# Performance work log

Hardware: AMD Instinct MI355X
Metric: run time of the kernel (lower is better)

Reference implementation:

```python
import jax, jax.numpy as jnp
import numpy as np

# Synthetic kinematic tree: 1 root + C0 chains of L0 atoms (generation 0 scans,
# rooted at node 0) + C1 branches of L1 atoms rooted mid-chain (generation 1 scans).
C0, L0 = 2048, 768
C1, L1 = 2048, 256
N = 1 + C0 * L0 + C1 * L1  # 2_097_153 atoms (incl. virtual root)


def setup_inputs() -> dict:
    key = jax.random.key(0)
    dofs = jax.random.normal(key, (N, 9), dtype=jnp.float32)

    chain_starts = 1 + np.arange(C0, dtype=np.int64) * L0          # first atom of each chain
    gen0 = np.concatenate(
        [np.zeros((C0, 1), np.int64),
         chain_starts[:, None] + np.arange(L0)[None, :]], axis=1)    # [C0, L0+1], col0 = root

    branch_roots = chain_starts + L0 // 2                            # computed during gen 0
    boff = 1 + C0 * L0
    gen1 = np.concatenate(
        [branch_roots[:, None],
         boff + (np.arange(C1, dtype=np.int64) * L1)[:, None] + np.arange(L1)[None, :]],
        axis=1)                                                      # [C1, L1+1]

    doftype = np.full((N,), 2, np.int32)  # BOND
    doftype[0] = 0                        # ROOT
    doftype[chain_starts] = 1             # JUMP at each chain start

    # kintree.id[1:] -> coords index: a fixed permutation (irregular scatter)
    id_idx = np.random.default_rng(0).permutation(N - 1).astype(np.int32)

    return {
        "dofs": dofs,
        "doftype": jnp.asarray(doftype),
        "gen0_paths": jnp.asarray(gen0, dtype=jnp.int32),
        "gen1_paths": jnp.asarray(gen1, dtype=jnp.int32),
        "id_idx": jnp.asarray(id_idx),
    }


def _rx(a):
    c, s = jnp.cos(a), jnp.sin(a)
    o, z = jnp.ones_like(a), jnp.zeros_like(a)
    return jnp.stack([jnp.stack([o, z, z, z], -1),
                      jnp.stack([z, c, -s, z], -1),
                      jnp.stack([z, s, c, z], -1),
                      jnp.stack([z, z, z, o], -1)], -2)


def _ry(a):
    c, s = jnp.cos(a), jnp.sin(a)
    o, z = jnp.ones_like(a), jnp.zeros_like(a)
    return jnp.stack([jnp.stack([c, z, s, z], -1),
                      jnp.stack([z, o, z, z], -1),
                      jnp.stack([-s, z, c, z], -1),
                      jnp.stack([z, z, z, o], -1)], -2)


def _rz(a):
    c, s = jnp.cos(a), jnp.sin(a)
    o, z = jnp.ones_like(a), jnp.zeros_like(a)
    return jnp.stack([jnp.stack([c, -s, z, z], -1),
                      jnp.stack([s, c, z, z], -1),
                      jnp.stack([z, z, o, z], -1),
                      jnp.stack([z, z, z, o], -1)], -2)


def _trans(x, y, z):
    o, zr = jnp.ones_like(x), jnp.zeros_like(x)
    return jnp.stack([jnp.stack([o, zr, zr, x], -1),
                      jnp.stack([zr, o, zr, y], -1),
                      jnp.stack([zr, zr, o, z], -1),
                      jnp.stack([zr, zr, zr, o], -1)], -2)


def _local_hts(dofs, doftype):
    # BOND dofs: phi_p, theta, d, phi_c  (NeRF-style internal coordinates)
    phi_p, theta, d, phi_c = dofs[:, 0], dofs[:, 1], dofs[:, 2], dofs[:, 3]
    z = jnp.zeros_like(d)
    bond = _rx(phi_p) @ _rz(jnp.pi - theta) @ _trans(d, z, z) @ _rx(phi_c)
    # JUMP dofs: RBx,RBy,RBz, RBdel_(a,b,c), RB_(a,b,c)
    rot = lambda a, b, c: _rz(c) @ _ry(b) @ _rx(a)
    jump = (_trans(dofs[:, 0], dofs[:, 1], dofs[:, 2])
            @ rot(dofs[:, 3], dofs[:, 4], dofs[:, 5])
            @ rot(dofs[:, 6], dofs[:, 7], dofs[:, 8]))
    eye = jnp.broadcast_to(jnp.eye(4, dtype=dofs.dtype), bond.shape)
    dt = doftype[:, None, None]
    return jnp.where(dt == 1, jump, jnp.where(dt == 2, bond, eye))


def reference(dofs, doftype, gen0_paths, gen1_paths, id_idx):
    hts = _local_hts(dofs, doftype)  # [N, 4, 4] local HTs; root = identity
    # Generation-ordered segmented scan: within each generation, each scan path's
    # first node already holds its GLOBAL HT; compose child = parent @ local along
    # the path via an associative prefix-matmul, then scatter back.
    for paths in (gen0_paths, gen1_paths):
        seg = hts[paths]                                        # [S, Lp, 4, 4]
        scanned = jax.lax.associative_scan(jnp.matmul, seg, axis=1)
        hts = hts.at[paths].set(scanned)
    kincoords = hts[:, :3, 3]                                   # [N, 3]
    coords = jnp.zeros((N - 1, 3), dtype=dofs.dtype)
    coords = coords.at[id_idx].set(kincoords[1:])               # coords[id[1:]] = kincoords[1:]
    return coords
```

## Files before the change

kernel.cpp:

```cpp
#include <hip/hip_runtime.h>
#include <math.h>

#define NC0 2048
#define NL0 768
#define NL1 256
#define BOFF (1 + NC0 * NL0)

struct Aff { float f[12]; };

__device__ __forceinline__ Aff affIdentity() {
    Aff M;
    M.f[0]=1.f; M.f[1]=0.f; M.f[2]=0.f;
    M.f[3]=0.f; M.f[4]=1.f; M.f[5]=0.f;
    M.f[6]=0.f; M.f[7]=0.f; M.f[8]=1.f;
    M.f[9]=0.f; M.f[10]=0.f; M.f[11]=0.f;
    return M;
}

__device__ __forceinline__ Aff compose(const Aff& A, const Aff& B) {
    Aff C;
#pragma unroll
    for (int i = 0; i < 3; ++i) {
        const float a0 = A.f[i*3+0], a1 = A.f[i*3+1], a2 = A.f[i*3+2];
#pragma unroll
        for (int j = 0; j < 3; ++j)
            C.f[i*3+j] = a0*B.f[0*3+j] + a1*B.f[1*3+j] + a2*B.f[2*3+j];
        C.f[9+i] = a0*B.f[9] + a1*B.f[10] + a2*B.f[11] + A.f[9+i];
    }
    return C;
}

__device__ __forceinline__ Aff shflUpA(const Aff& A, int d) {
    Aff B;
#pragma unroll
    for (int k = 0; k < 12; ++k) B.f[k] = __shfl_up(A.f[k], d, 64);
    return B;
}

__device__ __forceinline__ void fsc(float a, float& s, float& c) {
    s = __sinf(a);
    c = __cosf(a);
}

__device__ __forceinline__ Aff bondHT(float phi_p, float theta, float dd, float phi_c) {
    float sp, cp, st, ct, sc, cc;
    fsc(phi_p, sp, cp);
    fsc(theta, st, ct);
    fsc(phi_c, sc, cc);
    const float ca = -ct, sa = st;
    const float r00 = ca,    r01 = -sa;
    const float r10 = cp*sa, r11 = cp*ca,  r12 = -sp;
    const float r20 = sp*sa, r21 = sp*ca,  r22 = cp;
    Aff M;
    M.f[0] = r00; M.f[1] = r01*cc;          M.f[2] = -r01*sc;
    M.f[3] = r10; M.f[4] = r11*cc + r12*sc; M.f[5] = -r11*sc + r12*cc;
    M.f[6] = r20; M.f[7] = r21*cc + r22*sc; M.f[8] = -r21*sc + r22*cc;
    M.f[9] = r00*dd; M.f[10] = r10*dd; M.f[11] = r20*dd;
    return M;
}

__device__ __forceinline__ void rot3(float a, float b, float c, float* R) {
    float sa, ca, sb, cb, sg, cg;
    fsc(a, sa, ca);
    fsc(b, sb, cb);
    fsc(c, sg, cg);
    R[0] = cb*cg; R[1] = sa*sb*cg - ca*sg; R[2] = ca*sb*cg + sa*sg;
    R[3] = cb*sg; R[4] = sa*sb*sg + ca*cg; R[5] = ca*sb*sg - sa*cg;
    R[6] = -sb;   R[7] = sa*cb;            R[8] = ca*cb;
}

__device__ __forceinline__ Aff jumpHT(float d0, float d1, float d2,
                                      float d3, float d4, float d5,
                                      float d6, float d7, float d8) {
    float R1[9], R2[9];
    rot3(d3, d4, d5, R1);
    rot3(d6, d7, d8, R2);
    Aff M;
#pragma unroll
    for (int i = 0; i < 3; ++i)
#pragma unroll
        for (int j = 0; j < 3; ++j)
            M.f[i*3+j] = R1[i*3+0]*R2[0*3+j] + R1[i*3+1]*R2[1*3+j] + R1[i*3+2]*R2[2*3+j];
    M.f[9] = d0; M.f[10] = d1; M.f[11] = d2;
    return M;
}

__device__ __forceinline__ float f4c(const float4 v, int j) {
    return j == 0 ? v.x : j == 1 ? v.y : j == 2 ? v.z : v.w;
}
__device__ __forceinline__ int i4c(const int4 v, int j) {
    return j == 0 ? v.x : j == 1 ? v.y : j == 2 ? v.z : v.w;
}

#define GFA(m) f4c(ch[((m)+1)>>2], ((m)+1)&3)
#define GFB(m) f4c(chb[((m)+1)>>2], ((m)+1)&3)

__global__ __launch_bounds__(64)
void kin_kernel(const float* __restrict__ dofs,
                const int* __restrict__ id_idx,
                float* __restrict__ out) {
    const int c = blockIdx.x;
    const int t = threadIdx.x;

    const int ib0 = c * NL0 + 12 * t;
    const int4 i0 = *(const int4*)(id_idx + ib0 + 0);
    const int4 i1 = *(const int4*)(id_idx + ib0 + 4);
    const int4 i2 = *(const int4*)(id_idx + ib0 + 8);
    const int4 ibv = *(const int4*)(id_idx + (BOFF - 1) + c * NL1 + 4 * t);

    const float4* g4 = (const float4*)dofs;
    const size_t f0  = (size_t)(1 + c * NL0 + 12 * t) * 9;
    const size_t cb0 = (f0 - 1) >> 2;
    float4 ch[26];
    ch[0]  = g4[cb0 + 0];  ch[1]  = g4[cb0 + 1];  ch[2]  = g4[cb0 + 2];
    ch[3]  = g4[cb0 + 3];  ch[4]  = g4[cb0 + 4];  ch[5]  = g4[cb0 + 5];
    ch[7]  = g4[cb0 + 7];  ch[9]  = g4[cb0 + 9];  ch[10] = g4[cb0 + 10];
    ch[11] = g4[cb0 + 11]; ch[12] = g4[cb0 + 12]; ch[13] = g4[cb0 + 13];
    ch[14] = g4[cb0 + 14]; ch[16] = g4[cb0 + 16]; ch[18] = g4[cb0 + 18];
    ch[19] = g4[cb0 + 19]; ch[20] = g4[cb0 + 20]; ch[21] = g4[cb0 + 21];
    ch[22] = g4[cb0 + 22]; ch[23] = g4[cb0 + 23]; ch[25] = g4[cb0 + 25];

    const size_t f1  = (size_t)(BOFF + c * NL1 + 4 * t) * 9;
    const size_t cb1 = (f1 - 1) >> 2;
    float4 chb[8];
    chb[0] = g4[cb1 + 0]; chb[1] = g4[cb1 + 1]; chb[2] = g4[cb1 + 2];
    chb[3] = g4[cb1 + 3]; chb[4] = g4[cb1 + 4]; chb[5] = g4[cb1 + 5];
    chb[7] = g4[cb1 + 7];

    float qx[12], qy[12], qz[12];
    Aff Q, H0f;
#pragma unroll
    for (int k = 0; k < 12; ++k) {
        Aff H;
        if (k == 0) {
            if (t == 0)
                H = jumpHT(GFA(0), GFA(1), GFA(2), GFA(3), GFA(4),
                           GFA(5), GFA(6), GFA(7), GFA(8));
            else
                H = bondHT(GFA(0), GFA(1), GFA(2), GFA(3));
            H0f = H;
            Q = H;
        } else {
            H = bondHT(GFA(9*k+0), GFA(9*k+1), GFA(9*k+2), GFA(9*k+3));
            Q = compose(Q, H);
        }
        qx[k] = Q.f[9]; qy[k] = Q.f[10]; qz[k] = Q.f[11];
    }

    Aff S = Q;
#pragma unroll
    for (int s = 1; s < 64; s <<= 1) {
        const Aff P = shflUpA(S, s);
        if (t >= s) S = compose(P, S);
    }
    Aff E = shflUpA(S, 1);
    if (t == 0) E = affIdentity();

#pragma unroll
    for (int k = 0; k < 12; ++k) {
        const int oi = (k < 4) ? i4c(i0, k) : (k < 8) ? i4c(i1, k - 4) : i4c(i2, k - 8);
        float* o = out + (size_t)oi * 3;
        o[0] = E.f[0]*qx[k] + E.f[1]*qy[k] + E.f[2]*qz[k] + E.f[9];
        o[1] = E.f[3]*qx[k] + E.f[4]*qy[k] + E.f[5]*qz[k] + E.f[10];
        o[2] = E.f[6]*qx[k] + E.f[7]*qy[k] + E.f[8]*qz[k] + E.f[11];
    }

    Aff G = compose(E, H0f);
#pragma unroll
    for (int j = 0; j < 12; ++j) G.f[j] = __shfl(G.f[j], 32, 64);

    float rx[4], ry[4], rz[4];
    Aff R;
#pragma unroll
    for (int k = 0; k < 4; ++k) {
        const Aff Hb = bondHT(GFB(9*k+0), GFB(9*k+1), GFB(9*k+2), GFB(9*k+3));
        R = (k == 0) ? Hb : compose(R, Hb);
        rx[k] = R.f[9]; ry[k] = R.f[10]; rz[k] = R.f[11];
    }

    Aff Sb = R;
#pragma unroll
    for (int s = 1; s < 64; s <<= 1) {
        const Aff P = shflUpA(Sb, s);
        if (t >= s) Sb = compose(P, Sb);
    }
    Aff E1 = shflUpA(Sb, 1);
    if (t == 0) E1 = affIdentity();

    const Aff M = compose(G, E1);
#pragma unroll
    for (int k = 0; k < 4; ++k) {
        const int oi = i4c(ibv, k);
        float* o = out + (size_t)oi * 3;
        o[0] = M.f[0]*rx[k] + M.f[1]*ry[k] + M.f[2]*rz[k] + M.f[9];
        o[1] = M.f[3]*rx[k] + M.f[4]*ry[k] + M.f[5]*rz[k] + M.f[10];
        o[2] = M.f[6]*rx[k] + M.f[7]*ry[k] + M.f[8]*rz[k] + M.f[11];
    }
}

extern "C" void kernel_launch(void* const* d_in, const int* in_sizes, int n_in,
                              void* d_out, int out_size, void* d_ws, size_t ws_size,
                              hipStream_t stream) {
    const float* dofs   = (const float*)d_in[0];
    const int*   id_idx = (const int*)d_in[4];
    float*       out    = (float*)d_out;

    hipLaunchKernelGGL(kin_kernel, dim3(NC0), dim3(64), 0, stream,
                       dofs, id_idx, out);
}
```

Baseline: 163.5 us.

## Split each chain across two waves with LDS carry and interleaved scans

Each block now runs 128 threads (two waves), and each thread handles 6 chain atoms and 2 branch atoms instead of 12 and 4. The two wave-level scans for the chain and the branch are interleaved in one shuffle loop. Wave 0's totals pass to wave 1 through shared memory behind a block barrier. The branch root is rebuilt from wave 0's total times the bond at atom 384, so the broadcast from lane 32 is gone. The aim is to shorten each thread's serial chain and raise parallelism and occupancy, at the cost of a __syncthreads, extra composes, and narrower float2 loads.

```diff
diff --git a/kernel.cpp b/kernel.cpp
--- a/kernel.cpp
+++ b/kernel.cpp
@@ -85,52 +85,68 @@
     return M;
 }
 
-__device__ __forceinline__ float f4c(const float4 v, int j) {
-    return j == 0 ? v.x : j == 1 ? v.y : j == 2 ? v.z : v.w;
-}
-__device__ __forceinline__ int i4c(const int4 v, int j) {
-    return j == 0 ? v.x : j == 1 ? v.y : j == 2 ? v.z : v.w;
-}
-
-#define GFA(m) f4c(ch[((m)+1)>>2], ((m)+1)&3)
-#define GFB(m) f4c(chb[((m)+1)>>2], ((m)+1)&3)
-
-__global__ __launch_bounds__(64)
+__device__ __forceinline__ float f2c(const float2 v, int j) { return j ? v.y : v.x; }
+
+__device__ __forceinline__ void stA12(float* p, const Aff& A) {
+#pragma unroll
+    for (int k = 0; k < 12; ++k) p[k] = A.f[k];
+}
+__device__ __forceinline__ Aff ldA12(const float* p) {
+    Aff A;
+#pragma unroll
+    for (int k = 0; k < 12; ++k) A.f[k] = p[k];
+    return A;
+}
+
+#define GFA(m) f2c(ca[((m)+1)>>1], ((m)+1)&1)
+#define GFB(m) f2c(cb[((m)+1)>>1], ((m)+1)&1)
+#define GFR(m) f2c(cr[((m)+1)>>1], ((m)+1)&1)
+
+__global__ __launch_bounds__(128, 4)
 void kin_kernel(const float* __restrict__ dofs,
                 const int* __restrict__ id_idx,
                 float* __restrict__ out) {
-    const int c = blockIdx.x;
-    const int t = threadIdx.x;
-
-    const int ib0 = c * NL0 + 12 * t;
-    const int4 i0 = *(const int4*)(id_idx + ib0 + 0);
-    const int4 i1 = *(const int4*)(id_idx + ib0 + 4);
-    const int4 i2 = *(const int4*)(id_idx + ib0 + 8);
-    const int4 ibv = *(const int4*)(id_idx + (BOFF - 1) + c * NL1 + 4 * t);
-
-    const float4* g4 = (const float4*)dofs;
-    const size_t f0  = (size_t)(1 + c * NL0 + 12 * t) * 9;
-    const size_t cb0 = (f0 - 1) >> 2;
-    float4 ch[26];
-    ch[0]  = g4[cb0 + 0];  ch[1]  = g4[cb0 + 1];  ch[2]  = g4[cb0 + 2];
-    ch[3]  = g4[cb0 + 3];  ch[4]  = g4[cb0 + 4];  ch[5]  = g4[cb0 + 5];
-    ch[7]  = g4[cb0 + 7];  ch[9]  = g4[cb0 + 9];  ch[10] = g4[cb0 + 10];
-    ch[11] = g4[cb0 + 11]; ch[12] = g4[cb0 + 12]; ch[13] = g4[cb0 + 13];
-    ch[14] = g4[cb0 + 14]; ch[16] = g4[cb0 + 16]; ch[18] = g4[cb0 + 18];
-    ch[19] = g4[cb0 + 19]; ch[20] = g4[cb0 + 20]; ch[21] = g4[cb0 + 21];
-    ch[22] = g4[cb0 + 22]; ch[23] = g4[cb0 + 23]; ch[25] = g4[cb0 + 25];
-
-    const size_t f1  = (size_t)(BOFF + c * NL1 + 4 * t) * 9;
-    const size_t cb1 = (f1 - 1) >> 2;
-    float4 chb[8];
-    chb[0] = g4[cb1 + 0]; chb[1] = g4[cb1 + 1]; chb[2] = g4[cb1 + 2];
-    chb[3] = g4[cb1 + 3]; chb[4] = g4[cb1 + 4]; chb[5] = g4[cb1 + 5];
-    chb[7] = g4[cb1 + 7];
-
-    float qx[12], qy[12], qz[12];
-    Aff Q, H0f;
-#pragma unroll
-    for (int k = 0; k < 12; ++k) {
+    __shared__ float wt0[12];
+    __shared__ float wt1[12];
+
+    const int c    = blockIdx.x;
+    const int t    = threadIdx.x;
+    const int lane = t & 63;
+    const int wave = t >> 6;
+
+    const int ob0 = c * NL0 + 6 * t;
+    const int2 j0 = *(const int2*)(id_idx + ob0 + 0);
+    const int2 j1 = *(const int2*)(id_idx + ob0 + 2);
+    const int2 j2 = *(const int2*)(id_idx + ob0 + 4);
+    const int2 jb = *(const int2*)(id_idx + (BOFF - 1) + c * NL1 + 2 * t);
+
+    const float2* g2 = (const float2*)dofs;
+    const size_t f0 = (size_t)9 * (1 + (size_t)c * NL0 + 6 * t);
+    const size_t p0 = (f0 - 1) >> 1;
+    float2 ca[25];
+    ca[0]  = g2[p0+0];  ca[1]  = g2[p0+1];  ca[2]  = g2[p0+2];
+    ca[3]  = g2[p0+3];  ca[4]  = g2[p0+4];
+    ca[5]  = g2[p0+5];  ca[6]  = g2[p0+6];
+    ca[9]  = g2[p0+9];  ca[10] = g2[p0+10]; ca[11] = g2[p0+11];
+    ca[14] = g2[p0+14]; ca[15] = g2[p0+15];
+    ca[18] = g2[p0+18]; ca[19] = g2[p0+19]; ca[20] = g2[p0+20];
+    ca[23] = g2[p0+23]; ca[24] = g2[p0+24];
+
+    const size_t f1 = (size_t)9 * ((size_t)BOFF + (size_t)c * NL1 + 2 * t);
+    const size_t p1 = (f1 - 1) >> 1;
+    float2 cb[7];
+    cb[0] = g2[p1+0]; cb[1] = g2[p1+1]; cb[2] = g2[p1+2];
+    cb[5] = g2[p1+5]; cb[6] = g2[p1+6];
+
+    const size_t fr = (size_t)9 * (1 + (size_t)c * NL0 + 384);
+    const size_t pr = (fr - 1) >> 1;
+    float2 cr[3];
+    cr[0] = g2[pr+0]; cr[1] = g2[pr+1]; cr[2] = g2[pr+2];
+
+    float qx[6], qy[6], qz[6];
+    Aff Q;
+#pragma unroll
+    for (int k = 0; k < 6; ++k) {
         Aff H;
         if (k == 0) {
             if (t == 0)
@@ -138,7 +154,6 @@
                            GFA(5), GFA(6), GFA(7), GFA(8));
             else
                 H = bondHT(GFA(0), GFA(1), GFA(2), GFA(3));
-            H0f = H;
             Q = H;
         } else {
             H = bondHT(GFA(9*k+0), GFA(9*k+1), GFA(9*k+2), GFA(9*k+3));
@@ -147,50 +162,54 @@
         qx[k] = Q.f[9]; qy[k] = Q.f[10]; qz[k] = Q.f[11];
     }
 
+    float rx[2], ry[2], rz[2];
+    Aff R0 = bondHT(GFB(0), GFB(1), GFB(2), GFB(3));
+    rx[0] = R0.f[9]; ry[0] = R0.f[10]; rz[0] = R0.f[11];
+    Aff Sb = compose(R0, bondHT(GFB(9), GFB(10), GFB(11), GFB(12)));
+    rx[1] = Sb.f[9]; ry[1] = Sb.f[10]; rz[1] = Sb.f[11];
+
     Aff S = Q;
 #pragma unroll
     for (int s = 1; s < 64; s <<= 1) {
-        const Aff P = shflUpA(S, s);
-        if (t >= s) S = compose(P, S);
-    }
+        const Aff A = shflUpA(S, s);
+        const Aff B = shflUpA(Sb, s);
+        if (lane >= s) {
+            S  = compose(A, S);
+            Sb = compose(B, Sb);
+        }
+    }
+    if (wave == 0 && lane == 63) { stA12(wt0, S); stA12(wt1, Sb); }
+    __syncthreads();
+
+    const Aff W0 = ldA12(wt0);
+    const Aff W1 = ldA12(wt1);
+
     Aff E = shflUpA(S, 1);
-    if (t == 0) E = affIdentity();
-
-#pragma unroll
-    for (int k = 0; k < 12; ++k) {
-        const int oi = (k < 4) ? i4c(i0, k) : (k < 8) ? i4c(i1, k - 4) : i4c(i2, k - 8);
+    if (lane == 0) E = affIdentity();
+    const Aff EW = wave ? compose(W0, E) : E;
+
+#pragma unroll
+    for (int k = 0; k < 6; ++k) {
+        const int oi = (k < 2) ? (k ? j0.y : j0.x)
+                     : (k < 4) ? (k == 3 ? j1.y : j1.x)
+                               : (k == 5 ? j2.y : j2.x);
         float* o = out + (size_t)oi * 3;
-        o[0] = E.f[0]*qx[k] + E.f[1]*qy[k] + E.f[2]*qz[k] + E.f[9];
-        o[1] = E.f[3]*qx[k] + E.f[4]*qy[k] + E.f[5]*qz[k] + E.f[10];
-        o[2] = E.f[6]*qx[k] + E.f[7]*qy[k] + E.f[8]*qz[k] + E.f[11];
-    }
-
-    Aff G = compose(E, H0f);
-#pragma unroll
-    for (int j = 0; j < 12; ++j) G.f[j] = __shfl(G.f[j], 32, 64);
-
-    float rx[4], ry[4], rz[4];
-    Aff R;
-#pragma unroll
-    for (int k = 0; k < 4; ++k) {
-        const Aff Hb = bondHT(GFB(9*k+0), GFB(9*k+1), GFB(9*k+2), GFB(9*k+3));
-        R = (k == 0) ? Hb : compose(R, Hb);
-        rx[k] = R.f[9]; ry[k] = R.f[10]; rz[k] = R.f[11];
-    }
-
-    Aff Sb = R;
-#pragma unroll
-    for (int s = 1; s < 64; s <<= 1) {
-        const Aff P = shflUpA(Sb, s);
-        if (t >= s) Sb = compose(P, Sb);
-    }
+        o[0] = EW.f[0]*qx[k] + EW.f[1]*qy[k] + EW.f[2]*qz[k] + EW.f[9];
+        o[1] = EW.f[3]*qx[k] + EW.f[4]*qy[k] + EW.f[5]*qz[k] + EW.f[10];
+        o[2] = EW.f[6]*qx[k] + EW.f[7]*qy[k] + EW.f[8]*qz[k] + EW.f[11];
+    }
+
+    const Aff H384 = bondHT(GFR(0), GFR(1), GFR(2), GFR(3));
+    const Aff ROOT = compose(W0, H384);
+
     Aff E1 = shflUpA(Sb, 1);
-    if (t == 0) E1 = affIdentity();
-
-    const Aff M = compose(G, E1);
-#pragma unroll
-    for (int k = 0; k < 4; ++k) {
-        const int oi = i4c(ibv, k);
+    if (lane == 0) E1 = affIdentity();
+    const Aff RW1 = compose(ROOT, W1);
+    const Aff M = wave ? compose(RW1, E1) : compose(ROOT, E1);
+
+#pragma unroll
+    for (int k = 0; k < 2; ++k) {
+        const int oi = k ? jb.y : jb.x;
         float* o = out + (size_t)oi * 3;
         o[0] = M.f[0]*rx[k] + M.f[1]*ry[k] + M.f[2]*rz[k] + M.f[9];
         o[1] = M.f[3]*rx[k] + M.f[4]*ry[k] + M.f[5]*rz[k] + M.f[10];
@@ -205,6 +224,6 @@
     const int*   id_idx = (const int*)d_in[4];
     float*       out    = (float*)d_out;
 
-    hipLaunchKernelGGL(kin_kernel, dim3(NC0), dim3(64), 0, stream,
+    hipLaunchKernelGGL(kin_kernel, dim3(NC0), dim3(128), 0, stream,
                        dofs, id_idx, out);
 }
```

Result: slower. 177.4 us (+8.5%).
